# Kernel optimization log

Hardware: AMD Instinct MI355X
Metric: run time of the kernel (lower is better)

## Reference

```python
import jax, jax.numpy as jnp
import numpy as np
import math

B, S, E, H = 2, 2048, 1024, 16


def setup_inputs() -> dict:
    key = jax.random.key(0)
    ks = jax.random.split(key, 9)
    std = 0.02
    return {
        "x": jax.random.normal(ks[0], (B, S, E), dtype=jnp.float32),
        "Wq": jax.random.normal(ks[1], (E, E), dtype=jnp.float32) * std,
        "bq": jnp.zeros((E,), dtype=jnp.float32),
        "Wk": jax.random.normal(ks[2], (E, E), dtype=jnp.float32) * std,
        "bk": jnp.zeros((E,), dtype=jnp.float32),
        "Wv": jax.random.normal(ks[3], (E, E), dtype=jnp.float32) * std,
        "bv": jnp.zeros((E,), dtype=jnp.float32),
        "Wfc": jax.random.normal(ks[4], (E, E), dtype=jnp.float32) * std,
        "bfc": jnp.zeros((E,), dtype=jnp.float32),
        "n_head": H,
    }


def reference(x, Wq, bq, Wk, bk, Wv, bv, Wfc, bfc, n_head):
    Bn, Sn, En = x.shape
    Hd = En // n_head  # head_dim
    # torch Linear: y = x @ W.T + b
    def proj(W, b):
        return (x @ W.T + b).reshape(Bn, Sn, n_head, Hd).transpose(0, 2, 1, 3)  # [B,H,S,D]
    q = proj(Wq, bq)
    k = proj(Wk, bk)
    v = proj(Wv, bv)
    scores = jnp.einsum('bhqd,bhkd->bhqk', q, k) / math.sqrt(Hd)  # [B,H,S,S]
    # ALiBi: slopes_h = 2^{-(h+1)}; alibi[h,i,j] = -slope_h * (i - j)
    slopes = 2.0 ** (-jnp.arange(1, n_head + 1, dtype=jnp.float32))  # [H]
    pos = jnp.arange(Sn, dtype=jnp.float32)
    rel = pos[:, None] - pos[None, :]  # [S,S], memory_pos - context_pos
    alibi = -slopes[:, None, None] * rel  # [H,S,S]
    scores = scores + alibi[None]
    weights = jax.nn.softmax(scores, axis=-1)  # [B,H,S,S]
    out = jnp.einsum('bhqk,bhkd->bqhd', weights, v).reshape(Bn, Sn, En)
    out = out @ Wfc.T + bfc
    return (out, weights)
```

## Files before the change

kernel.cpp:

```cpp
#include <hip/hip_runtime.h>
#include <hip/hip_bf16.h>
#include <cstdint>
#include <cstddef>

#define BB 2
#define SS 2048
#define EE 1024
#define HH 16
#define MM (BB*SS)

typedef __bf16 bf16;
typedef __bf16 bf16x2 __attribute__((ext_vector_type(2)));
typedef __bf16 bf16x8 __attribute__((ext_vector_type(8)));
typedef float f32x4 __attribute__((ext_vector_type(4)));

#define GLD16(gsrc, ldst) \
  __builtin_amdgcn_global_load_lds((const __attribute__((address_space(1))) void*)(gsrc), \
                                   (__attribute__((address_space(3))) void*)(ldst), 16, 0, 0)

__global__ __launch_bounds__(256) void cvt_f32_bf16(const float* __restrict__ src,
                                                    bf16* __restrict__ dst, int n) {
    int i = (blockIdx.x * 256 + threadIdx.x) * 8;
    if (i >= n) return;
    float4 a = *(const float4*)(src + i);
    float4 b = *(const float4*)(src + i + 4);
    bf16 o[8] = {(bf16)a.x,(bf16)a.y,(bf16)a.z,(bf16)a.w,
                 (bf16)b.x,(bf16)b.y,(bf16)b.z,(bf16)b.w};
    *(uint4*)(dst + i) = *(uint4*)o;
}

__global__ __launch_bounds__(256) void cvt4(const float* __restrict__ a, const float* __restrict__ b,
                                            const float* __restrict__ c, const float* __restrict__ d,
                                            bf16* __restrict__ oa, bf16* __restrict__ ob,
                                            bf16* __restrict__ oc, bf16* __restrict__ od) {
    int sel = blockIdx.y;
    const float* s = sel == 0 ? a : sel == 1 ? b : sel == 2 ? c : d;
    bf16* o       = sel == 0 ? oa : sel == 1 ? ob : sel == 2 ? oc : od;
    int i = (blockIdx.x * 256 + threadIdx.x) * 8;
    float4 x = *(const float4*)(s + i);
    float4 y = *(const float4*)(s + i + 4);
    bf16 t[8] = {(bf16)x.x,(bf16)x.y,(bf16)x.z,(bf16)x.w,
                 (bf16)y.x,(bf16)y.y,(bf16)y.z,(bf16)y.w};
    *(uint4*)(o + i) = *(uint4*)t;
}

template<int MODE>
__global__ __launch_bounds__(256) void gemm128(const bf16* __restrict__ A,
                                               const bf16* __restrict__ W0,
                                               const bf16* __restrict__ W1,
                                               const bf16* __restrict__ W2,
                                               const float* __restrict__ b0,
                                               const float* __restrict__ b1,
                                               const float* __restrict__ b2,
                                               void* __restrict__ o0,
                                               void* __restrict__ o1,
                                               void* __restrict__ o2) {
    __shared__ bf16 Al[128*64];
    __shared__ bf16 Bl[128*64];
    const int t = threadIdx.x;
    const int wsel = blockIdx.x >> 3;
    const int n0 = (blockIdx.x & 7) * 128;
    const int m0 = blockIdx.y * 128;
    const bf16* W  = wsel == 0 ? W0 : wsel == 1 ? W1 : W2;
    const float* bias = wsel == 0 ? b0 : wsel == 1 ? b1 : b2;
    void* outp = wsel == 0 ? o0 : wsel == 1 ? o1 : o2;

    const int w = t >> 6, lane = t & 63, lg = lane >> 4, li = lane & 15;
    const int wr = w >> 1, wc = w & 1;
    f32x4 acc[4][4] = {};

    for (int k0 = 0; k0 < 1024; k0 += 64) {
        __syncthreads();
        #pragma unroll
        for (int i = 0; i < 4; ++i) {
            int f = i * 256 + t;
            int row = f >> 3, c = (f & 7) * 8;
            GLD16(A + (size_t)(m0 + row) * 1024 + k0 + c, Al + f * 8);
            GLD16(W + (size_t)(n0 + row) * 1024 + k0 + c, Bl + f * 8);
        }
        __syncthreads();
        #pragma unroll
        for (int ks = 0; ks < 2; ++ks) {
            bf16x8 af[4], bf_[4];
            #pragma unroll
            for (int m = 0; m < 4; ++m)
                af[m] = *(const bf16x8*)&Al[(wr*64 + m*16 + li)*64 + ks*32 + lg*8];
            #pragma unroll
            for (int n = 0; n < 4; ++n)
                bf_[n] = *(const bf16x8*)&Bl[(wc*64 + n*16 + li)*64 + ks*32 + lg*8];
            #pragma unroll
            for (int m = 0; m < 4; ++m)
                #pragma unroll
                for (int n = 0; n < 4; ++n)
                    acc[m][n] = __builtin_amdgcn_mfma_f32_16x16x32_bf16(af[m], bf_[n], acc[m][n], 0,0,0);
        }
    }
    #pragma unroll
    for (int m = 0; m < 4; ++m)
      #pragma unroll
      for (int n = 0; n < 4; ++n)
        #pragma unroll
        for (int r = 0; r < 4; ++r) {
            int row = m0 + wr*64 + m*16 + lg*4 + r;
            int col = n0 + wc*64 + n*16 + li;
            float v = acc[m][n][r] + bias[col];
            if (MODE == 0) {
                int b = row >> 11, s = row & (SS-1);
                int h = col >> 6, d = col & 63;
                ((bf16*)outp)[(((size_t)(b*HH + h)*SS + s) << 6) + d] = (bf16)v;
            } else {
                ((float*)outp)[(size_t)row*1024 + col] = v;
            }
        }
}

__global__ __launch_bounds__(256) void transpose_v(const bf16* __restrict__ V,
                                                   bf16* __restrict__ Vt) {
    __shared__ bf16 L[64][72];
    const int bh = blockIdx.y, s0 = blockIdx.x * 64, t = threadIdx.x;
    for (int id = t; id < 512; id += 256) {
        int row = id >> 3, c = id & 7;
        *(uint4*)&L[row][c*8] = *(const uint4*)&V[((size_t)bh*SS + s0 + row)*64 + c*8];
    }
    __syncthreads();
    for (int id = t; id < 512; id += 256) {
        int d = id >> 3, c = id & 7;
        bf16 tmp[8];
        #pragma unroll
        for (int jj = 0; jj < 8; ++jj) tmp[jj] = L[c*8 + jj][d];
        *(uint4*)&Vt[((size_t)bh*64 + d)*SS + s0 + c*8] = *(uint4*)tmp;
    }
}

__global__ __launch_bounds__(256) void attn_kernel(const bf16* __restrict__ Q,
                                                   const bf16* __restrict__ Kk,
                                                   const bf16* __restrict__ Vt,
                                                   float* __restrict__ wout,
                                                   bf16* __restrict__ aout) {
    __shared__ bf16 Ks[2][64*64];
    __shared__ bf16 Vs[2][64*64];
    __shared__ bf16 Ps[64*64];
    char* Psb = (char*)Ps;

    const int qt = blockIdx.x, bh = blockIdx.y;
    const int b = bh >> 4, h = bh & 15;
    const int q0 = qt * 64;
    const int t = threadIdx.x, w = t >> 6, lane = t & 63, lg = lane >> 4, li = lane & 15;
    const float slope = exp2f(-(float)(h + 1));
    const size_t kvbase = (size_t)bh * SS * 64;
    const size_t vtbase = (size_t)bh * 64 * SS;
    const float L2E = 1.4426950408889634f;
    const float K1 = 0.125f * L2E;
    const float C  = slope * L2E;
    const float C64 = C * 64.f;

    const bf16* qptr = Q + kvbase + (size_t)(q0 + w*16 + li) * 64;
    bf16x8 aq0 = *(const bf16x8*)(qptr + lg*8);
    bf16x8 aq1 = *(const bf16x8*)(qptr + 32 + lg*8);

    const int swz = (li & 7) << 4;
    float ecr[4][4];
    #pragma unroll
    for (int cb = 0; cb < 4; ++cb)
        #pragma unroll
        for (int r = 0; r < 4; ++r)
            ecr[cb][r] = C * (float)(cb*16 + lg*4 + r - (SS-1));

    float l = 0.f;

    #pragma unroll
    for (int i = 0; i < 2; ++i) {
        int f = i*256 + t; int row = f >> 3, c16 = f & 7;
        GLD16(Kk + kvbase + (size_t)row*64 + (c16 ^ (row & 7))*8, &Ks[0][0] + f*8);
    }
    __syncthreads();
    for (int kt = 0; kt < 32; ++kt) {
        const int cur = kt & 1;
        if (kt + 1 < 32) {
            #pragma unroll
            for (int i = 0; i < 2; ++i) {
                int f = i*256 + t; int row = f >> 3, c16 = f & 7;
                GLD16(Kk + kvbase + (size_t)((kt+1)*64 + row)*64 + (c16 ^ (row & 7))*8,
                      &Ks[cur^1][0] + f*8);
            }
        }
        const char* Ksb = (const char*)&Ks[cur][0];
        f32x4 sc[4] = {};
        #pragma unroll
        for (int cb = 0; cb < 4; ++cb) {
            int row = cb*16 + li;
            bf16x8 bk0 = *(const bf16x8*)(Ksb + row*128 + ((     lg*16) ^ swz));
            bf16x8 bk1 = *(const bf16x8*)(Ksb + row*128 + ((64 + lg*16) ^ swz));
            sc[cb] = __builtin_amdgcn_mfma_f32_16x16x32_bf16(bk0, aq0, sc[cb], 0,0,0);
            sc[cb] = __builtin_amdgcn_mfma_f32_16x16x32_bf16(bk1, aq1, sc[cb], 0,0,0);
        }
        #pragma unroll
        for (int cb = 0; cb < 4; ++cb)
            #pragma unroll
            for (int r = 0; r < 4; ++r) {
                l += __builtin_amdgcn_exp2f(fmaf(sc[cb][r], K1, ecr[cb][r]));
                ecr[cb][r] += C64;
            }
        __syncthreads();
    }
    l += __shfl_xor(l, 16);
    l += __shfl_xor(l, 32);
    const float lgl = __builtin_amdgcn_logf(l);

    #pragma unroll
    for (int cb = 0; cb < 4; ++cb)
        #pragma unroll
        for (int r = 0; r < 4; ++r)
            ecr[cb][r] = C * (float)(cb*16 + lg*4 + r - (SS-1)) - lgl;

    f32x4 acc[4] = {};
    float* wrow = wout + ((size_t)bh*SS + q0 + w*16 + li) * SS;
    const int prow = w*16 + li;

    #pragma unroll
    for (int i = 0; i < 2; ++i) {
        int f = i*256 + t; int row = f >> 3, c16 = f & 7;
        GLD16(Kk + kvbase + (size_t)row*64 + (c16 ^ (row & 7))*8, &Ks[0][0] + f*8);
        GLD16(Vt + vtbase + (size_t)row*SS + (c16 ^ (row & 7))*8, &Vs[0][0] + f*8);
    }
    __syncthreads();
    for (int kt = 0; kt < 32; ++kt) {
        const int cur = kt & 1;
        const int j0 = kt * 64;
        if (kt + 1 < 32) {
            #pragma unroll
            for (int i = 0; i < 2; ++i) {
                int f = i*256 + t; int row = f >> 3, c16 = f & 7;
                GLD16(Kk + kvbase + (size_t)(j0 + 64 + row)*64 + (c16 ^ (row & 7))*8,
                      &Ks[cur^1][0] + f*8);
                GLD16(Vt + vtbase + (size_t)row*SS + j0 + 64 + (c16 ^ (row & 7))*8,
                      &Vs[cur^1][0] + f*8);
            }
        }
        const char* Ksb = (const char*)&Ks[cur][0];
        const char* Vsb = (const char*)&Vs[cur][0];
        f32x4 sc[4] = {};
        #pragma unroll
        for (int cb = 0; cb < 4; ++cb) {
            int row = cb*16 + li;
            bf16x8 bk0 = *(const bf16x8*)(Ksb + row*128 + ((     lg*16) ^ swz));
            bf16x8 bk1 = *(const bf16x8*)(Ksb + row*128 + ((64 + lg*16) ^ swz));
            sc[cb] = __builtin_amdgcn_mfma_f32_16x16x32_bf16(bk0, aq0, sc[cb], 0,0,0);
            sc[cb] = __builtin_amdgcn_mfma_f32_16x16x32_bf16(bk1, aq1, sc[cb], 0,0,0);
        }
        #pragma unroll
        for (int cb = 0; cb < 4; ++cb) {
            float4 wv;
            wv.x = __builtin_amdgcn_exp2f(fmaf(sc[cb][0], K1, ecr[cb][0]));
            wv.y = __builtin_amdgcn_exp2f(fmaf(sc[cb][1], K1, ecr[cb][1]));
            wv.z = __builtin_amdgcn_exp2f(fmaf(sc[cb][2], K1, ecr[cb][2]));
            wv.w = __builtin_amdgcn_exp2f(fmaf(sc[cb][3], K1, ecr[cb][3]));
            *(float4*)&wrow[j0 + cb*16 + lg*4] = wv;
            bf16x2 p01 = {(bf16)wv.x, (bf16)wv.y};
            bf16x2 p23 = {(bf16)wv.z, (bf16)wv.w};
            uint2 u;
            u.x = __builtin_bit_cast(unsigned, p01);
            u.y = __builtin_bit_cast(unsigned, p23);
            *(uint2*)(Psb + prow*128 + ((cb*32 + lg*8) ^ swz)) = u;
            ecr[cb][0] += C64; ecr[cb][1] += C64;
            ecr[cb][2] += C64; ecr[cb][3] += C64;
        }
        #pragma unroll
        for (int ks = 0; ks < 2; ++ks) {
            bf16x8 ap = *(const bf16x8*)(Psb + prow*128 + ((ks*64 + lg*16) ^ swz));
            #pragma unroll
            for (int d0 = 0; d0 < 4; ++d0) {
                int vrow = d0*16 + li;
                bf16x8 bv = *(const bf16x8*)(Vsb + vrow*128 + ((ks*64 + lg*16) ^ swz));
                acc[d0] = __builtin_amdgcn_mfma_f32_16x16x32_bf16(ap, bv, acc[d0], 0,0,0);
            }
        }
        __syncthreads();
    }
    #pragma unroll
    for (int d0 = 0; d0 < 4; ++d0)
        #pragma unroll
        for (int r = 0; r < 4; ++r) {
            int srow = q0 + w*16 + lg*4 + r;
            aout[((size_t)(b*SS + srow))*EE + h*64 + d0*16 + li] = (bf16)acc[d0][r];
        }
}

extern "C" void kernel_launch(void* const* d_in, const int* in_sizes, int n_in,
                              void* d_out, int out_size, void* d_ws, size_t ws_size,
                              hipStream_t stream) {
    const float* x   = (const float*)d_in[0];
    const float* Wq  = (const float*)d_in[1];
    const float* bq  = (const float*)d_in[2];
    const float* Wk  = (const float*)d_in[3];
    const float* bk  = (const float*)d_in[4];
    const float* Wv  = (const float*)d_in[5];
    const float* bv  = (const float*)d_in[6];
    const float* Wfc = (const float*)d_in[7];
    const float* bfc = (const float*)d_in[8];

    char* ws = (char*)d_ws;
    const size_t MB = 1024u*1024u;
    bf16* xb  = (bf16*)(ws + 0);
    bf16* wqb = (bf16*)(ws + 8*MB);
    bf16* wkb = (bf16*)(ws + 10*MB);
    bf16* wvb = (bf16*)(ws + 12*MB);
    bf16* wfb = (bf16*)(ws + 14*MB);
    bf16* Qb  = (bf16*)(ws + 16*MB);
    bf16* Kb  = (bf16*)(ws + 24*MB);
    bf16* Vb  = (bf16*)(ws + 32*MB);
    bf16* Vtb = (bf16*)(ws + 40*MB);
    bf16* Ab  = (bf16*)(ws + 48*MB);

    float* outp = (float*)d_out;
    float* wout = outp + (size_t)BB*SS*EE;

    cvt_f32_bf16<<<dim3(4194304/8/256), 256, 0, stream>>>(x, xb, 4194304);
    cvt4<<<dim3(512, 4), 256, 0, stream>>>(Wq, Wk, Wv, Wfc, wqb, wkb, wvb, wfb);

    gemm128<0><<<dim3(24, 32), 256, 0, stream>>>(xb, wqb, wkb, wvb, bq, bk, bv, Qb, Kb, Vb);

    transpose_v<<<dim3(SS/64, BB*HH), 256, 0, stream>>>(Vb, Vtb);

    attn_kernel<<<dim3(SS/64, BB*HH), 256, 0, stream>>>(Qb, Kb, Vtb, wout, Ab);

    gemm128<1><<<dim3(8, 32), 256, 0, stream>>>(Ab, wfb, wfb, wfb, bfc, bfc, bfc, d_out, d_out, d_out);
}
```

Baseline: 298.3 us.

## Split attention tile into 2x2 warp grid over query and key halves

Each warp now handles 32 query rows and half of each 64-key tile, rather than 16 query rows across all keys. This lets the P fragment feed the PV MFMA straight from registers, removing the shared-memory P round trip, and lets each K fragment be reused across two query blocks. Row sums and partial outputs from the two key halves are combined through shared memory at the end, which adds a reduction and an extra bf16 rounding step. It also remaps block indices for L2 locality and raises wave priority around the MFMA sections.

```diff
diff --git a/kernel.cpp b/kernel.cpp
--- a/kernel.cpp
+++ b/kernel.cpp
@@ -10,7 +10,6 @@
 #define MM (BB*SS)
 
 typedef __bf16 bf16;
-typedef __bf16 bf16x2 __attribute__((ext_vector_type(2)));
 typedef __bf16 bf16x8 __attribute__((ext_vector_type(8)));
 typedef float f32x4 __attribute__((ext_vector_type(4)));
 
@@ -139,13 +138,16 @@
                                                    bf16* __restrict__ aout) {
     __shared__ bf16 Ks[2][64*64];
     __shared__ bf16 Vs[2][64*64];
-    __shared__ bf16 Ps[64*64];
-    char* Psb = (char*)Ps;
-
-    const int qt = blockIdx.x, bh = blockIdx.y;
+    __shared__ float Lred[2][64];
+
+    const int lin = blockIdx.x + (int)(gridDim.x * blockIdx.y);
+    const int nl  = (lin & 7) * 128 + (lin >> 3);
+    const int qt = nl & 31, bh = nl >> 5;
+
     const int b = bh >> 4, h = bh & 15;
     const int q0 = qt * 64;
     const int t = threadIdx.x, w = t >> 6, lane = t & 63, lg = lane >> 4, li = lane & 15;
+    const int jh = w & 1, qh = w >> 1;
     const float slope = exp2f(-(float)(h + 1));
     const size_t kvbase = (size_t)bh * SS * 64;
     const size_t vtbase = (size_t)bh * 64 * SS;
@@ -154,19 +156,23 @@
     const float C  = slope * L2E;
     const float C64 = C * 64.f;
 
-    const bf16* qptr = Q + kvbase + (size_t)(q0 + w*16 + li) * 64;
-    bf16x8 aq0 = *(const bf16x8*)(qptr + lg*8);
-    bf16x8 aq1 = *(const bf16x8*)(qptr + 32 + lg*8);
+    bf16x8 aq[2][2];
+    #pragma unroll
+    for (int cbq = 0; cbq < 2; ++cbq) {
+        const bf16* qptr = Q + kvbase + (size_t)(q0 + qh*32 + cbq*16 + li) * 64;
+        aq[cbq][0] = *(const bf16x8*)(qptr + lg*8);
+        aq[cbq][1] = *(const bf16x8*)(qptr + 32 + lg*8);
+    }
 
     const int swz = (li & 7) << 4;
-    float ecr[4][4];
-    #pragma unroll
-    for (int cb = 0; cb < 4; ++cb)
+
+    float cj[2][4];
+    #pragma unroll
+    for (int jt = 0; jt < 2; ++jt)
         #pragma unroll
         for (int r = 0; r < 4; ++r)
-            ecr[cb][r] = C * (float)(cb*16 + lg*4 + r - (SS-1));
-
-    float l = 0.f;
+            cj[jt][r] = C * (float)(jh*32 + jt*16 + lg*4 + r - (SS-1));
+    float lp[2] = {0.f, 0.f};
 
     #pragma unroll
     for (int i = 0; i < 2; ++i) {
@@ -185,38 +191,44 @@
             }
         }
         const char* Ksb = (const char*)&Ks[cur][0];
-        f32x4 sc[4] = {};
-        #pragma unroll
-        for (int cb = 0; cb < 4; ++cb) {
-            int row = cb*16 + li;
-            bf16x8 bk0 = *(const bf16x8*)(Ksb + row*128 + ((     lg*16) ^ swz));
-            bf16x8 bk1 = *(const bf16x8*)(Ksb + row*128 + ((64 + lg*16) ^ swz));
-            sc[cb] = __builtin_amdgcn_mfma_f32_16x16x32_bf16(bk0, aq0, sc[cb], 0,0,0);
-            sc[cb] = __builtin_amdgcn_mfma_f32_16x16x32_bf16(bk1, aq1, sc[cb], 0,0,0);
-        }
-        #pragma unroll
-        for (int cb = 0; cb < 4; ++cb)
-            #pragma unroll
-            for (int r = 0; r < 4; ++r) {
-                l += __builtin_amdgcn_exp2f(fmaf(sc[cb][r], K1, ecr[cb][r]));
-                ecr[cb][r] += C64;
-            }
+        bf16x8 ak[2][2];
+        #pragma unroll
+        for (int jt = 0; jt < 2; ++jt) {
+            int row = jh*32 + jt*16 + li;
+            ak[jt][0] = *(const bf16x8*)(Ksb + row*128 + ((     lg*16) ^ swz));
+            ak[jt][1] = *(const bf16x8*)(Ksb + row*128 + ((64 + lg*16) ^ swz));
+        }
+        f32x4 sc[2][2] = {};
+        __builtin_amdgcn_s_setprio(1);
+        #pragma unroll
+        for (int jt = 0; jt < 2; ++jt)
+            #pragma unroll
+            for (int cbq = 0; cbq < 2; ++cbq) {
+                sc[jt][cbq] = __builtin_amdgcn_mfma_f32_16x16x32_bf16(ak[jt][0], aq[cbq][0], sc[jt][cbq], 0,0,0);
+                sc[jt][cbq] = __builtin_amdgcn_mfma_f32_16x16x32_bf16(ak[jt][1], aq[cbq][1], sc[jt][cbq], 0,0,0);
+            }
+        __builtin_amdgcn_s_setprio(0);
+        #pragma unroll
+        for (int jt = 0; jt < 2; ++jt) {
+            #pragma unroll
+            for (int cbq = 0; cbq < 2; ++cbq)
+                #pragma unroll
+                for (int r = 0; r < 4; ++r)
+                    lp[cbq] += __builtin_amdgcn_exp2f(fmaf(sc[jt][cbq][r], K1, cj[jt][r]));
+            #pragma unroll
+            for (int r = 0; r < 4; ++r) cj[jt][r] += C64;
+        }
         __syncthreads();
     }
-    l += __shfl_xor(l, 16);
-    l += __shfl_xor(l, 32);
-    const float lgl = __builtin_amdgcn_logf(l);
-
-    #pragma unroll
-    for (int cb = 0; cb < 4; ++cb)
-        #pragma unroll
-        for (int r = 0; r < 4; ++r)
-            ecr[cb][r] = C * (float)(cb*16 + lg*4 + r - (SS-1)) - lgl;
-
-    f32x4 acc[4] = {};
-    float* wrow = wout + ((size_t)bh*SS + q0 + w*16 + li) * SS;
-    const int prow = w*16 + li;
-
+    #pragma unroll
+    for (int cbq = 0; cbq < 2; ++cbq) {
+        lp[cbq] += __shfl_xor(lp[cbq], 16);
+        lp[cbq] += __shfl_xor(lp[cbq], 32);
+    }
+    if (lg == 0) {
+        Lred[jh][qh*32 + li]      = lp[0];
+        Lred[jh][qh*32 + 16 + li] = lp[1];
+    }
     #pragma unroll
     for (int i = 0; i < 2; ++i) {
         int f = i*256 + t; int row = f >> 3, c16 = f & 7;
@@ -224,6 +236,25 @@
         GLD16(Vt + vtbase + (size_t)row*SS + (c16 ^ (row & 7))*8, &Vs[0][0] + f*8);
     }
     __syncthreads();
+    float lgl[2];
+    #pragma unroll
+    for (int cbq = 0; cbq < 2; ++cbq) {
+        int qi = qh*32 + cbq*16 + li;
+        lgl[cbq] = __builtin_amdgcn_logf(Lred[0][qi] + Lred[1][qi]);
+    }
+    float ecr[2][2][4];
+    #pragma unroll
+    for (int jt = 0; jt < 2; ++jt)
+        #pragma unroll
+        for (int cbq = 0; cbq < 2; ++cbq)
+            #pragma unroll
+            for (int r = 0; r < 4; ++r)
+                ecr[jt][cbq][r] = C * (float)(jh*32 + jt*16 + lg*4 + r - (SS-1)) - lgl[cbq];
+
+    f32x4 acc[2][4] = {};
+    float* wrow0 = wout + ((size_t)bh*SS + q0 + qh*32 +      li) * SS;
+    float* wrow1 = wout + ((size_t)bh*SS + q0 + qh*32 + 16 + li) * SS;
+
     for (int kt = 0; kt < 32; ++kt) {
         const int cur = kt & 1;
         const int j0 = kt * 64;
@@ -239,51 +270,94 @@
         }
         const char* Ksb = (const char*)&Ks[cur][0];
         const char* Vsb = (const char*)&Vs[cur][0];
-        f32x4 sc[4] = {};
-        #pragma unroll
-        for (int cb = 0; cb < 4; ++cb) {
-            int row = cb*16 + li;
-            bf16x8 bk0 = *(const bf16x8*)(Ksb + row*128 + ((     lg*16) ^ swz));
-            bf16x8 bk1 = *(const bf16x8*)(Ksb + row*128 + ((64 + lg*16) ^ swz));
-            sc[cb] = __builtin_amdgcn_mfma_f32_16x16x32_bf16(bk0, aq0, sc[cb], 0,0,0);
-            sc[cb] = __builtin_amdgcn_mfma_f32_16x16x32_bf16(bk1, aq1, sc[cb], 0,0,0);
-        }
-        #pragma unroll
-        for (int cb = 0; cb < 4; ++cb) {
-            float4 wv;
-            wv.x = __builtin_amdgcn_exp2f(fmaf(sc[cb][0], K1, ecr[cb][0]));
-            wv.y = __builtin_amdgcn_exp2f(fmaf(sc[cb][1], K1, ecr[cb][1]));
-            wv.z = __builtin_amdgcn_exp2f(fmaf(sc[cb][2], K1, ecr[cb][2]));
-            wv.w = __builtin_amdgcn_exp2f(fmaf(sc[cb][3], K1, ecr[cb][3]));
-            *(float4*)&wrow[j0 + cb*16 + lg*4] = wv;
-            bf16x2 p01 = {(bf16)wv.x, (bf16)wv.y};
-            bf16x2 p23 = {(bf16)wv.z, (bf16)wv.w};
-            uint2 u;
-            u.x = __builtin_bit_cast(unsigned, p01);
-            u.y = __builtin_bit_cast(unsigned, p23);
-            *(uint2*)(Psb + prow*128 + ((cb*32 + lg*8) ^ swz)) = u;
-            ecr[cb][0] += C64; ecr[cb][1] += C64;
-            ecr[cb][2] += C64; ecr[cb][3] += C64;
-        }
-        #pragma unroll
-        for (int ks = 0; ks < 2; ++ks) {
-            bf16x8 ap = *(const bf16x8*)(Psb + prow*128 + ((ks*64 + lg*16) ^ swz));
-            #pragma unroll
-            for (int d0 = 0; d0 < 4; ++d0) {
-                int vrow = d0*16 + li;
-                bf16x8 bv = *(const bf16x8*)(Vsb + vrow*128 + ((ks*64 + lg*16) ^ swz));
-                acc[d0] = __builtin_amdgcn_mfma_f32_16x16x32_bf16(ap, bv, acc[d0], 0,0,0);
-            }
-        }
+        bf16x8 ak[2][2];
+        #pragma unroll
+        for (int jt = 0; jt < 2; ++jt) {
+            int row = jh*32 + jt*16 + li;
+            ak[jt][0] = *(const bf16x8*)(Ksb + row*128 + ((     lg*16) ^ swz));
+            ak[jt][1] = *(const bf16x8*)(Ksb + row*128 + ((64 + lg*16) ^ swz));
+        }
+        f32x4 sc[2][2] = {};
+        __builtin_amdgcn_s_setprio(1);
+        #pragma unroll
+        for (int jt = 0; jt < 2; ++jt)
+            #pragma unroll
+            for (int cbq = 0; cbq < 2; ++cbq) {
+                sc[jt][cbq] = __builtin_amdgcn_mfma_f32_16x16x32_bf16(ak[jt][0], aq[cbq][0], sc[jt][cbq], 0,0,0);
+                sc[jt][cbq] = __builtin_amdgcn_mfma_f32_16x16x32_bf16(ak[jt][1], aq[cbq][1], sc[jt][cbq], 0,0,0);
+            }
+        __builtin_amdgcn_s_setprio(0);
+        float4 wv[2][2];
+        #pragma unroll
+        for (int jt = 0; jt < 2; ++jt)
+            #pragma unroll
+            for (int cbq = 0; cbq < 2; ++cbq) {
+                float4 v;
+                v.x = __builtin_amdgcn_exp2f(fmaf(sc[jt][cbq][0], K1, ecr[jt][cbq][0]));
+                v.y = __builtin_amdgcn_exp2f(fmaf(sc[jt][cbq][1], K1, ecr[jt][cbq][1]));
+                v.z = __builtin_amdgcn_exp2f(fmaf(sc[jt][cbq][2], K1, ecr[jt][cbq][2]));
+                v.w = __builtin_amdgcn_exp2f(fmaf(sc[jt][cbq][3], K1, ecr[jt][cbq][3]));
+                wv[jt][cbq] = v;
+                float* wr = (cbq == 0 ? wrow0 : wrow1);
+                *(float4*)&wr[j0 + jh*32 + jt*16 + lg*4] = v;
+                ecr[jt][cbq][0] += C64; ecr[jt][cbq][1] += C64;
+                ecr[jt][cbq][2] += C64; ecr[jt][cbq][3] += C64;
+            }
+        bf16x8 pa[2];
+        #pragma unroll
+        for (int cbq = 0; cbq < 2; ++cbq) {
+            bf16x8 p;
+            p[0] = (bf16)wv[0][cbq].x; p[1] = (bf16)wv[0][cbq].y;
+            p[2] = (bf16)wv[0][cbq].z; p[3] = (bf16)wv[0][cbq].w;
+            p[4] = (bf16)wv[1][cbq].x; p[5] = (bf16)wv[1][cbq].y;
+            p[6] = (bf16)wv[1][cbq].z; p[7] = (bf16)wv[1][cbq].w;
+            pa[cbq] = p;
+        }
+        bf16x8 vb[4];
+        #pragma unroll
+        for (int d0 = 0; d0 < 4; ++d0) {
+            int row = d0*16 + li;
+            uint2 u0 = *(const uint2*)(Vsb + row*128 + ((jh*64      + lg*8) ^ swz));
+            uint2 u1 = *(const uint2*)(Vsb + row*128 + ((jh*64 + 32 + lg*8) ^ swz));
+            uint4 uu = {u0.x, u0.y, u1.x, u1.y};
+            vb[d0] = __builtin_bit_cast(bf16x8, uu);
+        }
+        __builtin_amdgcn_s_setprio(1);
+        #pragma unroll
+        for (int cbq = 0; cbq < 2; ++cbq)
+            #pragma unroll
+            for (int d0 = 0; d0 < 4; ++d0)
+                acc[cbq][d0] = __builtin_amdgcn_mfma_f32_16x16x32_bf16(pa[cbq], vb[d0], acc[cbq][d0], 0,0,0);
+        __builtin_amdgcn_s_setprio(0);
         __syncthreads();
     }
-    #pragma unroll
-    for (int d0 = 0; d0 < 4; ++d0)
-        #pragma unroll
-        for (int r = 0; r < 4; ++r) {
-            int srow = q0 + w*16 + lg*4 + r;
-            aout[((size_t)(b*SS + srow))*EE + h*64 + d0*16 + li] = (bf16)acc[d0][r];
-        }
+
+    bf16* Obuf = &Ks[0][0];
+    #pragma unroll
+    for (int cbq = 0; cbq < 2; ++cbq)
+        #pragma unroll
+        for (int d0 = 0; d0 < 4; ++d0)
+            #pragma unroll
+            for (int r = 0; r < 4; ++r)
+                Obuf[jh*4096 + (qh*32 + cbq*16 + lg*4 + r)*64 + d0*16 + li] =
+                    (bf16)acc[cbq][d0][r];
+    __syncthreads();
+    {
+        int q = t >> 2, dc = (t & 3) << 4;
+        const bf16* o0 = Obuf +        q*64 + dc;
+        const bf16* o1 = Obuf + 4096 + q*64 + dc;
+        bf16x8 a0 = *(const bf16x8*)(o0),     a1 = *(const bf16x8*)(o0 + 8);
+        bf16x8 b0 = *(const bf16x8*)(o1),     b1 = *(const bf16x8*)(o1 + 8);
+        bf16 ov[16];
+        #pragma unroll
+        for (int e = 0; e < 8; ++e) {
+            ov[e]     = (bf16)((float)a0[e] + (float)b0[e]);
+            ov[8 + e] = (bf16)((float)a1[e] + (float)b1[e]);
+        }
+        bf16* dst = aout + ((size_t)(b*SS + q0 + q))*EE + h*64 + dc;
+        *(uint4*)(dst)     = *(uint4*)(ov);
+        *(uint4*)(dst + 8) = *(uint4*)(ov + 8);
+    }
 }
 
 extern "C" void kernel_launch(void* const* d_in, const int* in_sizes, int n_in,
@@ -322,7 +396,7 @@
 
     transpose_v<<<dim3(SS/64, BB*HH), 256, 0, stream>>>(Vb, Vtb);
 
-    attn_kernel<<<dim3(SS/64, BB*HH), 256, 0, stream>>>(Qb, Kb, Vtb, wout, Ab);
+    attn_kernel<<<dim3(32, 32), 256, 0, stream>>>(Qb, Kb, Vtb, wout, Ab);
 
     gemm128<1><<<dim3(8, 32), 256, 0, stream>>>(Ab, wfb, wfb, wfb, bfc, bfc, bfc, d_out, d_out, d_out);
 }
```

Result: slower. 307.3 us (+3.0%).
